# Kernel optimization log

Measured on AMD Instinct MI355X. Metric: run time of the kernel, lower is better.

## Reference

```python
import jax, jax.numpy as jnp
import numpy as np

BS, SL, NN, NE = 8, 100, 200, 600
C = 110; CP1 = C + 1
D = 128          # node_embed_dim
DC = 64          # concept_embed_dim
H = 256          # lstm hidden
VOCAB = 50000
NPROB = 1000
FEAT = 2 + CP1 + DC  # LSTM input dim = 177


def setup_inputs() -> dict:
    key = jax.random.key(0)
    ks = jax.random.split(key, 24)
    f32 = jnp.float32
    p_id = jax.random.randint(ks[0], (BS, SL), 0, NPROB)
    c_id = jax.random.bernoulli(ks[1], 0.1, (BS, SL, CP1)).astype(f32)
    node_id = jax.random.randint(ks[2], (BS, SL, NN), 0, VOCAB)
    edge = jax.random.randint(ks[3], (BS, SL, 2, NE), 0, NN)
    edge_type = jax.random.randint(ks[4], (BS, SL, NE), 0, 8)
    target_c = jax.random.bernoulli(ks[5], 0.05, (BS, SL, CP1)).astype(f32)
    target_c = target_c.at[:, :, 0].set(1.0)  # every step has >=1 target concept
    result = jax.random.bernoulli(ks[6], 0.5, (BS * SL, 1)).astype(f32)
    c_embed = jax.random.bernoulli(ks[7], 0.1, (BS, SL, CP1)).astype(f32)
    cur_result = jax.random.normal(ks[8], (BS, SL, 2), f32)
    # parameters
    node_embed_w = jax.random.normal(ks[9], (VOCAB, D), f32) * 0.02
    edge_embed_w = (jax.random.normal(ks[10], (8, D), f32) * 0.02).at[0].set(0.0)  # padding_idx=0
    ggnn_w = jax.random.normal(ks[11], (4, D, D), f32) * 0.05
    gru_w_ih = jax.random.normal(ks[12], (3 * D, D), f32) * 0.05
    gru_w_hh = jax.random.normal(ks[13], (3 * D, D), f32) * 0.05
    gru_b_ih = jnp.zeros((3 * D,), f32)
    gru_b_hh = jnp.zeros((3 * D,), f32)
    transdim_w = jax.random.normal(ks[14], (DC, D), f32) * 0.05
    concept_embedding = jax.random.normal(ks[15], (CP1, DC), f32) * 0.05
    lstm_w_ih = jax.random.normal(ks[16], (4 * H, FEAT), f32) * 0.05
    lstm_w_hh = jax.random.normal(ks[17], (4 * H, H), f32) * 0.05
    lstm_b_ih = jnp.zeros((4 * H,), f32)
    lstm_b_hh = jnp.zeros((4 * H,), f32)
    pred_w = jax.random.normal(ks[18], (CP1, H), f32) * 0.05
    pred_b = jnp.zeros((CP1,), f32)
    return dict(p_id=p_id, c_id=c_id, node_id=node_id, edge=edge, edge_type=edge_type,
                target_c=target_c, result=result, c_embed=c_embed, cur_result=cur_result,
                node_embed_w=node_embed_w, edge_embed_w=edge_embed_w, ggnn_w=ggnn_w,
                gru_w_ih=gru_w_ih, gru_w_hh=gru_w_hh, gru_b_ih=gru_b_ih, gru_b_hh=gru_b_hh,
                transdim_w=transdim_w, concept_embedding=concept_embedding,
                lstm_w_ih=lstm_w_ih, lstm_w_hh=lstm_w_hh, lstm_b_ih=lstm_b_ih,
                lstm_b_hh=lstm_b_hh, pred_w=pred_w, pred_b=pred_b)


def _forward(p_id, c_id, node_id, edge, edge_type, target_c, result, c_embed, cur_result,
             node_embed_w, edge_embed_w, ggnn_w, gru_w_ih, gru_w_hh, gru_b_ih, gru_b_hh,
             transdim_w, concept_embedding, lstm_w_ih, lstm_w_hh, lstm_b_ih, lstm_b_hh,
             pred_w, pred_b):
    bs, sl = p_id.shape
    N = node_id.shape[2]
    G = bs * sl  # all graphs batched (replaces torch per-sample python loop)
    x = node_embed_w[node_id].reshape(G, N, -1)                       # [G,N,D]
    ew = edge_embed_w[edge_type].mean(-1).reshape(G, -1, 1)           # [G,E,1]
    e = edge.reshape(G, 2, -1)
    src, dst = e[:, 0], e[:, 1]                                       # [G,E]
    flat_dst = (dst + jnp.arange(G)[:, None] * N).reshape(-1)
    d = x.shape[-1]
    # GatedGraphConv, 4 layers: m = x @ W_l, sum-aggregate edge_weight*m[src] at dst, GRUCell update
    for l in range(4):
        m = jnp.einsum('gnd,de->gne', x, ggnn_w[l])
        gathered = jnp.take_along_axis(m, src[:, :, None], axis=1)    # [G,E,D]
        msg = (ew * gathered).reshape(-1, d)
        agg = jax.ops.segment_sum(msg, flat_dst, num_segments=G * N).reshape(G, N, d)
        gi = agg @ gru_w_ih.T + gru_b_ih
        gh = x @ gru_w_hh.T + gru_b_hh
        i_r, i_z, i_n = jnp.split(gi, 3, axis=-1)
        h_r, h_z, h_n = jnp.split(gh, 3, axis=-1)
        r = jax.nn.sigmoid(i_r + h_r)
        z = jax.nn.sigmoid(i_z + h_z)
        n = jnp.tanh(i_n + r * h_n)
        x = (1.0 - z) * n + z * x
    # transdim (node_embed_dim != concept_embed_dim)
    ggnn = jnp.einsum('gnd,cd->gnc', x, transdim_w)                   # [G,N,DC]
    # concept-node attention
    ce = c_embed.reshape(G, -1, 1)                                    # [G,C+1,1]
    query = ce * concept_embedding[None]                              # [G,C+1,DC]
    attn_w = jax.nn.softmax(jnp.einsum('gcd,gnd->gcn', query, ggnn), axis=2)
    attn = jnp.einsum('gcn,gnd->gcd', attn_w, ggnn) * ce
    num = jnp.sum(c_id, axis=2).reshape(G, 1)
    num = jnp.where(num == 0, 1.0, num)
    attn_out = (jnp.sum(attn, axis=1) / num).reshape(bs, sl, -1)
    # LSTM (1 layer, batch_first)
    lstm_in = jnp.concatenate([c_embed, attn_out, cur_result], axis=2)
    hdim = pred_w.shape[1]
    def step(carry, xt):
        h, c = carry
        gates = xt @ lstm_w_ih.T + lstm_b_ih + h @ lstm_w_hh.T + lstm_b_hh
        i, f, g, o = jnp.split(gates, 4, axis=-1)
        c = jax.nn.sigmoid(f) * c + jax.nn.sigmoid(i) * jnp.tanh(g)
        h = jax.nn.sigmoid(o) * jnp.tanh(c)
        return (h, c), h
    init = (jnp.zeros((bs, hdim), lstm_in.dtype), jnp.zeros((bs, hdim), lstm_in.dtype))
    _, hs = jax.lax.scan(step, init, jnp.swapaxes(lstm_in, 0, 1))
    lstm_out = jnp.swapaxes(hs, 0, 1).reshape(G, hdim)
    # prediction + masked BCE-with-logits
    pred = lstm_out @ pred_w.T + pred_b                               # [G,C+1]
    tc = target_c.reshape(G, -1)
    pred1 = jnp.sum(pred * tc, axis=1)
    nc = jnp.sum(tc, axis=1)
    mask = nc > 0
    fp = pred1 / jnp.where(mask, nc, 1.0)
    ft = result.reshape(-1)
    bce = jnp.maximum(fp, 0.0) - fp * ft + jnp.log1p(jnp.exp(-jnp.abs(fp)))
    mf = mask.astype(fp.dtype)
    loss = jnp.sum(bce * mf) / jnp.maximum(jnp.sum(mf), 1.0)
    return loss, jax.nn.sigmoid(fp), ft


def reference(p_id, c_id, node_id, edge, edge_type, target_c, result, c_embed, cur_result,
              node_embed_w, edge_embed_w, ggnn_w, gru_w_ih, gru_w_hh, gru_b_ih, gru_b_hh,
              transdim_w, concept_embedding, lstm_w_ih, lstm_w_hh, lstm_b_ih, lstm_b_hh,
              pred_w, pred_b):
    return _forward(p_id, c_id, node_id, edge, edge_type, target_c, result, c_embed, cur_result,
                    node_embed_w, edge_embed_w, ggnn_w, gru_w_ih, gru_w_hh, gru_b_ih, gru_b_hh,
                    transdim_w, concept_embedding, lstm_w_ih, lstm_w_hh, lstm_b_ih, lstm_b_hh,
                    pred_w, pred_b)
```

## Files before the change

### kernel.cpp

```cpp
#include <hip/hip_runtime.h>
#include <math.h>

static const int BSZ   = 8;
static const int SLN   = 100;
static const int NNODE = 200;
static const int NEDGE = 600;
static const int CP1N  = 111;
static const int DIM   = 128;
static const int DCN   = 64;
static const int HID   = 256;
static const int FEATN = 177;
static const int GN    = 800;
static const int MROW  = 160000;

typedef unsigned short u16;
typedef u16    u16x8  __attribute__((ext_vector_type(8)));
typedef __bf16 bf16x8 __attribute__((ext_vector_type(8)));
typedef __bf16 bf16x2 __attribute__((ext_vector_type(2)));
typedef float  f32x16 __attribute__((ext_vector_type(16)));

#if defined(__has_builtin)
# if __has_builtin(__builtin_amdgcn_fdot2_f32_bf16)
#  define HAVE_FDOT2 1
# else
#  define HAVE_FDOT2 0
# endif
#else
# define HAVE_FDOT2 0
#endif

__device__ __forceinline__ float sigf(float v){ return 1.0f/(1.0f + expf(-v)); }
__device__ __forceinline__ u16 f2bf(float f){
    union { float f; unsigned u; } v; v.f = f;
    unsigned r = v.u + 0x7FFFu + ((v.u >> 16) & 1u);
    return (u16)(r >> 16);
}
__device__ __forceinline__ float bf2f(u16 u){
    union { unsigned u; float f; } v; v.u = ((unsigned)u) << 16;
    return v.f;
}
__device__ __forceinline__ float dot2bf(unsigned w, unsigned h, float acc){
#if HAVE_FDOT2
    return __builtin_amdgcn_fdot2_f32_bf16(__builtin_bit_cast(bf16x2, w),
                                           __builtin_bit_cast(bf16x2, h), acc, false);
#else
    acc += bf2f((u16)(w & 0xffffu)) * bf2f((u16)(h & 0xffffu));
    acc += bf2f((u16)(w >> 16))     * bf2f((u16)(h >> 16));
    return acc;
#endif
}

__device__ __forceinline__ int afrag_slot(int row, int kc8){
    int kcq = kc8 >> 1;
    int pos = (row & 31) + 32*(kc8 & 1);
    return ((row >> 5)*8 + kcq)*64 + (pos ^ kcq);
}

__global__ void k_transpose_w(const float* __restrict__ whh, const float* __restrict__ wih,
                              unsigned* __restrict__ whhP, float* __restrict__ wihT){
    int idx = blockIdx.x*blockDim.x + threadIdx.x;
    const int total1 = 128*1024;
    if (idx < total1){
        int k2 = idx >> 10, j = idx & 1023;
        u16 lo = f2bf(whh[(size_t)j*256 + 2*k2]);
        u16 hi = f2bf(whh[(size_t)j*256 + 2*k2 + 1]);
        whhP[(size_t)k2*1024 + j] = (unsigned)lo | ((unsigned)hi << 16);
    }
    int idx2 = idx - total1;
    const int total2 = FEATN*1024;
    if (idx2 >= 0 && idx2 < total2){
        int k = idx2 >> 10, j = idx2 & 1023;
        wihT[(size_t)k*1024 + j] = wih[(size_t)j*FEATN + k];
    }
}

__global__ void k_convert_w(const float* __restrict__ wih, const float* __restrict__ whh,
                            const float* __restrict__ gw, const float* __restrict__ tw,
                            u16* __restrict__ wihb, u16* __restrict__ whhb,
                            u16* __restrict__ gwTb, u16* __restrict__ twb){
    int idx = blockIdx.x*blockDim.x + threadIdx.x;
    if (idx < 49152){
        wihb[idx] = f2bf(wih[idx]);
    } else if (idx < 98304){
        int t = idx - 49152;
        whhb[t] = f2bf(whh[t]);
    } else if (idx < 163840){
        int t = idx - 98304;
        int l = t >> 14, rem = t & 16383, n = rem >> 7, k = rem & 127;
        gwTb[t] = f2bf(gw[((size_t)l*128 + k)*128 + n]);
    } else if (idx < 172032){
        int t = idx - 163840;
        twb[t] = f2bf(tw[t]);
    }
}

__global__ void __launch_bounds__(256)
k_build_csr(const int* __restrict__ edge, const int* __restrict__ etype,
            const float* __restrict__ eembed,
            int* __restrict__ csr_src, float* __restrict__ csr_w, int* __restrict__ csr_off){
    int g = blockIdx.x; int tid = threadIdx.x;
    __shared__ float tmean[8];
    __shared__ float tpart[8][32];
    __shared__ int cnt[NNODE];
    __shared__ int offs[NNODE+1];
    __shared__ int cur[NNODE];
    {
        int ty = tid >> 5, lane = tid & 31;
        float s = 0.f;
        for (int i = lane; i < DIM; i += 32) s += eembed[ty*DIM + i];
        tpart[ty][lane] = s;
    }
    for (int i = tid; i < NNODE; i += 256) cnt[i] = 0;
    __syncthreads();
    if (tid < 8){
        float s = 0.f;
        for (int i = 0; i < 32; i++) s += tpart[tid][i];
        tmean[tid] = s / (float)DIM;
    }
    for (int e = tid; e < NEDGE; e += 256){
        int dst = edge[((size_t)g*2+1)*NEDGE + e];
        atomicAdd(&cnt[dst], 1);
    }
    __syncthreads();
    if (tid == 0){
        int run = 0;
        for (int i = 0; i < NNODE; i++){ offs[i] = run; run += cnt[i]; }
        offs[NNODE] = run;
    }
    __syncthreads();
    for (int i = tid; i < NNODE; i += 256) cur[i] = offs[i];
    for (int i = tid; i < NNODE+1; i += 256) csr_off[(size_t)g*(NNODE+1)+i] = offs[i];
    __syncthreads();
    for (int e = tid; e < NEDGE; e += 256){
        int dst = edge[((size_t)g*2+1)*NEDGE + e];
        int src = edge[((size_t)g*2+0)*NEDGE + e];
        float w = tmean[etype[(size_t)g*NEDGE + e]];
        int pos = atomicAdd(&cur[dst], 1);
        csr_src[(size_t)g*NEDGE + pos] = src;
        csr_w [(size_t)g*NEDGE + pos] = w;
    }
}

__global__ void k_gather_x(const int* __restrict__ nid, const float4* __restrict__ emb,
                           u16x8* __restrict__ xb){
    const long total = (long)MROW*16;
    for (long c = (long)blockIdx.x*blockDim.x + threadIdx.x; c < total; c += (long)gridDim.x*blockDim.x){
        long row = c >> 4; int p = (int)(c & 15);
        float4 a = emb[(size_t)nid[row]*32 + p*2];
        float4 b = emb[(size_t)nid[row]*32 + p*2 + 1];
        u16x8 v;
        v[0]=f2bf(a.x); v[1]=f2bf(a.y); v[2]=f2bf(a.z); v[3]=f2bf(a.w);
        v[4]=f2bf(b.x); v[5]=f2bf(b.y); v[6]=f2bf(b.z); v[7]=f2bf(b.w);
        xb[c] = v;
    }
}

__global__ void __launch_bounds__(256)
k_mm_scatter(const u16* __restrict__ xb, const u16* __restrict__ gwTb_l,
             const int* __restrict__ csr_src, const float* __restrict__ csr_w,
             const int* __restrict__ csr_off, u16* __restrict__ aggb){
    __shared__ u16 smem[224*128];
    __shared__ int   e_src[NEDGE];
    __shared__ float e_w[NEDGE];
    __shared__ int   offs_s[NNODE+1];
    int g = blockIdx.x;
    int tid = threadIdx.x;
    const u16x8* xg = (const u16x8*)(xb + (size_t)g*NNODE*DIM);
    u16x8* afrag = (u16x8*)smem;
    for (int c = tid; c < 3584; c += 256){
        int row = c >> 4, kc8 = c & 15;
        u16x8 v = {};
        if (row < NNODE) v = xg[row*16 + kc8];
        afrag[afrag_slot(row, kc8)] = v;
    }
    {
        const int*   srcp = csr_src + (size_t)g*NEDGE;
        const float* wp   = csr_w   + (size_t)g*NEDGE;
        const int*   off  = csr_off + (size_t)g*(NNODE+1);
        for (int i = tid; i < NEDGE; i += 256){ e_src[i] = srcp[i]; e_w[i] = wp[i]; }
        for (int i = tid; i <= NNODE; i += 256) offs_s[i] = off[i];
    }
    __syncthreads();
    int w = tid >> 6, lane = tid & 63;
    int nbase = w*32;
    int m = lane & 31, kh = lane >> 5;
    f32x16 acc[7];
    #pragma unroll
    for (int t = 0; t < 7; t++) acc[t] = (f32x16)0.f;
    const u16x8* bp = (const u16x8*)gwTb_l;
    int nrow = nbase + m;
    #pragma unroll
    for (int kc = 0; kc < 8; kc++){
        u16x8 b = bp[nrow*16 + kc*2 + kh];
        #pragma unroll
        for (int mt = 0; mt < 7; mt++){
            u16x8 a = afrag[(mt*8 + kc)*64 + (lane ^ kc)];
            acc[mt] = __builtin_amdgcn_mfma_f32_32x32x16_bf16(
                __builtin_bit_cast(bf16x8, a), __builtin_bit_cast(bf16x8, b), acc[mt], 0, 0, 0);
        }
    }
    __syncthreads();
    #pragma unroll
    for (int mt = 0; mt < 7; mt++){
        #pragma unroll
        for (int r = 0; r < 16; r++){
            int row = mt*32 + (r&3) + 8*(r>>2) + 4*kh;
            int col = nbase + m;
            smem[row*128 + col] = f2bf(acc[mt][r]);
        }
    }
    __syncthreads();
    const unsigned* m32 = (const unsigned*)smem;
    int j2 = tid & 63, rg = tid >> 6;
    unsigned* aggout = (unsigned*)(aggb + (size_t)g*NNODE*DIM);
    for (int i = 0; i < 50; i++){
        int n = rg*50 + i;
        int b0 = offs_s[n], e0 = offs_s[n+1];
        float a0 = 0.f, a1 = 0.f;
        for (int p = b0; p < e0; p++){
            unsigned mv = m32[e_src[p]*64 + j2];
            float w_ = e_w[p];
            a0 += w_ * bf2f((u16)(mv & 0xffffu));
            a1 += w_ * bf2f((u16)(mv >> 16));
        }
        aggout[(size_t)n*64 + j2] = (unsigned)f2bf(a0) | ((unsigned)f2bf(a1) << 16);
    }
}

__global__ void __launch_bounds__(512, 2)
k_gru_mfma(u16* __restrict__ xb, const u16* __restrict__ aggb,
           const u16* __restrict__ wihb, const u16* __restrict__ whhb,
           const float* __restrict__ bih, const float* __restrict__ bhh){
    __shared__ u16x8 afragA[2048];
    __shared__ u16x8 afragX[2048];
    int tid = threadIdx.x;
    long r0 = (long)blockIdx.x * 128;
    const u16x8* aggp = (const u16x8*)aggb;
    const u16x8* xbp  = (const u16x8*)xb;
    for (int c = tid; c < 4096; c += 512){
        int mat = c >> 11, cc = c & 2047;
        int row = cc >> 4, kc8 = cc & 15;
        u16x8 v = (mat ? xbp : aggp)[(r0 + row)*16 + kc8];
        (mat ? afragX : afragA)[afrag_slot(row, kc8)] = v;
    }
    __syncthreads();
    int w = tid >> 6, lane = tid & 63;
    int mtg = w >> 2;
    int cb  = (w & 3) * 32;
    f32x16 acc0[6], acc1[6];
    #pragma unroll
    for (int t = 0; t < 6; t++){ acc0[t] = (f32x16)0.f; acc1[t] = (f32x16)0.f; }
    const u16x8* bi = (const u16x8*)wihb;
    const u16x8* bh = (const u16x8*)whhb;
    int kh = lane >> 5;
    int ncol = cb + (lane & 31);
    #pragma unroll
    for (int kc = 0; kc < 8; kc++){
        int lx = lane ^ kc;
        u16x8 aA0 = afragA[((2*mtg+0)*8 + kc)*64 + lx];
        u16x8 aA1 = afragA[((2*mtg+1)*8 + kc)*64 + lx];
        u16x8 aX0 = afragX[((2*mtg+0)*8 + kc)*64 + lx];
        u16x8 aX1 = afragX[((2*mtg+1)*8 + kc)*64 + lx];
        #pragma unroll
        for (int g3 = 0; g3 < 3; g3++){
            int n = g3*128 + ncol;
            u16x8 b1 = bi[n*16 + kc*2 + kh];
            u16x8 b2 = bh[n*16 + kc*2 + kh];
            acc0[g3]   = __builtin_amdgcn_mfma_f32_32x32x16_bf16(
                __builtin_bit_cast(bf16x8, aA0), __builtin_bit_cast(bf16x8, b1), acc0[g3], 0,0,0);
            acc1[g3]   = __builtin_amdgcn_mfma_f32_32x32x16_bf16(
                __builtin_bit_cast(bf16x8, aA1), __builtin_bit_cast(bf16x8, b1), acc1[g3], 0,0,0);
            acc0[3+g3] = __builtin_amdgcn_mfma_f32_32x32x16_bf16(
                __builtin_bit_cast(bf16x8, aX0), __builtin_bit_cast(bf16x8, b2), acc0[3+g3], 0,0,0);
            acc1[3+g3] = __builtin_amdgcn_mfma_f32_32x32x16_bf16(
                __builtin_bit_cast(bf16x8, aX1), __builtin_bit_cast(bf16x8, b2), acc1[3+g3], 0,0,0);
        }
    }
    int col = cb + (lane & 31);
    float bir = bih[col], biz = bih[col+128], bin = bih[col+256];
    float bhr = bhh[col], bhz = bhh[col+128], bhn = bhh[col+256];
    int kc8c = col >> 3, elc = col & 7;
    #pragma unroll
    for (int mt2 = 0; mt2 < 2; mt2++){
        const f32x16* ac = mt2 ? acc1 : acc0;
        #pragma unroll
        for (int r = 0; r < 16; r++){
            int row = mtg*64 + mt2*32 + (r&3) + 8*(r>>2) + 4*kh;
            u16x8 xv = afragX[afrag_slot(row, kc8c)];
            float xo = bf2f(((const u16*)&xv)[elc]);
            float rr  = sigf(ac[0][r] + bir + ac[3][r] + bhr);
            float zz  = sigf(ac[1][r] + biz + ac[4][r] + bhz);
            float nn_ = tanhf(ac[2][r] + bin + rr*(ac[5][r] + bhn));
            float xn  = (1.f - zz)*nn_ + zz*xo;
            xb[(size_t)(r0 + row)*DIM + col] = f2bf(xn);
        }
    }
}

__global__ void __launch_bounds__(256)
k_transdim(const u16* __restrict__ xb, const u16* __restrict__ twb, u16* __restrict__ out){
    int tid = threadIdx.x;
    int w = tid >> 6, lane = tid & 63;
    int m = lane & 31, kh = lane >> 5;
    long r0 = (long)blockIdx.x * 128;
    const u16x8* xp = (const u16x8*)xb;
    const u16x8* tp = (const u16x8*)twb;
    long rowA = r0 + w*32 + m;
    f32x16 acc[2];
    acc[0] = (f32x16)0.f; acc[1] = (f32x16)0.f;
    #pragma unroll
    for (int kc = 0; kc < 8; kc++){
        u16x8 a = xp[rowA*16 + kc*2 + kh];
        #pragma unroll
        for (int nt = 0; nt < 2; nt++){
            u16x8 b = tp[(nt*32 + m)*16 + kc*2 + kh];
            acc[nt] = __builtin_amdgcn_mfma_f32_32x32x16_bf16(
                __builtin_bit_cast(bf16x8, a), __builtin_bit_cast(bf16x8, b), acc[nt], 0,0,0);
        }
    }
    #pragma unroll
    for (int nt = 0; nt < 2; nt++){
        #pragma unroll
        for (int r = 0; r < 16; r++){
            int row = w*32 + (r&3) + 8*(r>>2) + 4*kh;
            int col = nt*32 + m;
            out[(r0 + row)*DCN + col] = f2bf(acc[nt][r]);
        }
    }
}

__global__ void __launch_bounds__(256)
k_attention(const u16* __restrict__ gout, const float* __restrict__ cemb,
            const float* __restrict__ cid, const float* __restrict__ conc,
            const float* __restrict__ curres, float* __restrict__ lstm_in){
    int g = blockIdx.x; int tid = threadIdx.x;
    int lane = tid & 63, wv = tid >> 6;
    __shared__ float gg[NNODE*65];
    __shared__ float ce_s[CP1N];
    __shared__ float sc[256];
    __shared__ float wredA[4];
    __shared__ float wredB[4];
    __shared__ float part[4][DCN];
    __shared__ float oacc[DCN];
    __shared__ float num_s;
    if (tid < CP1N) ce_s[tid] = cemb[(size_t)g*CP1N + tid];
    if (tid < DCN) oacc[tid] = 0.f;
    for (int i = tid; i < NNODE*DCN; i += 256){
        int n = i >> 6, d = i & 63;
        gg[n*65 + d] = bf2f(gout[(size_t)g*NNODE*DCN + i]);
    }
    {
        float v = (tid < CP1N) ? cid[(size_t)g*CP1N + tid] : 0.f;
        #pragma unroll
        for (int m2 = 32; m2; m2 >>= 1) v += __shfl_xor(v, m2);
        if (lane == 0) wredA[wv] = v;
    }
    __syncthreads();
    if (tid == 0){
        float nm = wredA[0]+wredA[1]+wredA[2]+wredA[3];
        num_s = (nm == 0.f) ? 1.f : nm;
    }
    __syncthreads();
    for (int c = 0; c < CP1N; c++){
        float ce = ce_s[c];
        if (ce == 0.f) continue;
        const float* qc = conc + c*DCN;
        float s = -1e30f;
        if (tid < NNODE){
            float a_ = 0.f;
            const float* gr_ = &gg[tid*65];
            #pragma unroll 16
            for (int d = 0; d < DCN; d++) a_ += qc[d] * gr_[d];
            s = ce * a_;
        }
        float m_ = s;
        #pragma unroll
        for (int m2 = 32; m2; m2 >>= 1) m_ = fmaxf(m_, __shfl_xor(m_, m2));
        if (lane == 0) wredA[wv] = m_;
        __syncthreads();
        float mx = fmaxf(fmaxf(wredA[0], wredA[1]), fmaxf(wredA[2], wredA[3]));
        float e = (tid < NNODE) ? expf(s - mx) : 0.f;
        sc[tid] = e;
        float sum_ = e;
        #pragma unroll
        for (int m2 = 32; m2; m2 >>= 1) sum_ += __shfl_xor(sum_, m2);
        if (lane == 0) wredB[wv] = sum_;
        __syncthreads();
        float inv = ce / (wredB[0]+wredB[1]+wredB[2]+wredB[3]);
        float pa = 0.f;
        for (int n = wv; n < NNODE; n += 4) pa += sc[n] * gg[n*65 + lane];
        part[wv][lane] = pa;
        __syncthreads();
        if (tid < DCN) oacc[tid] += inv * (part[0][tid] + part[1][tid] + part[2][tid] + part[3][tid]);
    }
    __syncthreads();
    if (tid < FEATN){
        float v;
        if      (tid < CP1N)       v = ce_s[tid];
        else if (tid < CP1N+DCN)   v = oacc[tid-CP1N] / num_s;
        else                       v = curres[(size_t)g*2 + (tid-CP1N-DCN)];
        lstm_in[(size_t)g*FEATN + tid] = v;
    }
}

__global__ void __launch_bounds__(256)
k_gi(const float* __restrict__ lstm_in, const float* __restrict__ wihT,
     const float* __restrict__ bih, const float* __restrict__ bhh, float* __restrict__ gi){
    int rb = blockIdx.x;
    int jb = blockIdx.y;
    int tid = threadIdx.x;
    __shared__ float in_s[8][FEATN];
    for (int i = tid; i < 8*FEATN; i += 256){ int r = i/FEATN, k = i%FEATN; in_s[r][k] = lstm_in[((size_t)rb*8+r)*FEATN + k]; }
    __syncthreads();
    int j = jb*256 + tid;
    float acc[8];
    #pragma unroll
    for (int i = 0; i < 8; i++) acc[i] = 0.f;
    for (int k = 0; k < FEATN; k++){
        float w = wihT[(size_t)k*1024 + j];
        #pragma unroll
        for (int i = 0; i < 8; i++) acc[i] += in_s[i][k] * w;
    }
    float b = bih[j] + bhh[j];
    #pragma unroll
    for (int i = 0; i < 8; i++) gi[((size_t)rb*8+i)*1024 + j] = acc[i] + b;
}

static const int WREG = 104;
static const int WL4  = 6;

__global__ void __launch_bounds__(1024)
__attribute__((amdgpu_waves_per_eu(4,4)))
k_lstm(const float* __restrict__ gi, const unsigned* __restrict__ whhP, float* __restrict__ out){
    int b = blockIdx.x; int tid = threadIdx.x;
    __shared__ uint4 ldsw4[WL4][1024];
    __shared__ float gates[1024];
    __shared__ __align__(8) u16 h16[HID];
    unsigned wreg[WREG];
    #pragma unroll
    for (int i = 0; i < WREG; i++) wreg[i] = whhP[(size_t)i*1024 + tid];
    #pragma unroll
    for (int q = 0; q < WL4; q++){
        uint4 v;
        v.x = whhP[(size_t)(WREG + 4*q + 0)*1024 + tid];
        v.y = whhP[(size_t)(WREG + 4*q + 1)*1024 + tid];
        v.z = whhP[(size_t)(WREG + 4*q + 2)*1024 + tid];
        v.w = whhP[(size_t)(WREG + 4*q + 3)*1024 + tid];
        ldsw4[q][tid] = v;
    }
    if (tid < 128) ((unsigned*)h16)[tid] = 0u;
    float c_reg = 0.f;
    int lane = tid & 63;
    __syncthreads();
    float giv = gi[(size_t)b*SLN*1024 + tid];
    for (int t = 0; t < SLN; t++){
        unsigned hv0 = ((const unsigned*)h16)[lane];
        unsigned hv1 = ((const unsigned*)h16)[64 + lane];
        float acc0 = giv, acc1 = 0.f;
        if (t+1 < SLN) giv = gi[((size_t)b*SLN + t + 1)*1024 + tid];
        #pragma unroll
        for (int p = 0; p < 64; p += 2){
            unsigned hpa = (unsigned)__builtin_amdgcn_readlane((int)hv0, p);
            unsigned hpb = (unsigned)__builtin_amdgcn_readlane((int)hv0, p+1);
            acc0 = dot2bf(wreg[p],   hpa, acc0);
            acc1 = dot2bf(wreg[p+1], hpb, acc1);
        }
        #pragma unroll
        for (int p = 64; p < WREG; p += 2){
            unsigned hpa = (unsigned)__builtin_amdgcn_readlane((int)hv1, p - 64);
            unsigned hpb = (unsigned)__builtin_amdgcn_readlane((int)hv1, p - 63);
            acc0 = dot2bf(wreg[p],   hpa, acc0);
            acc1 = dot2bf(wreg[p+1], hpb, acc1);
        }
        #pragma unroll
        for (int q = 0; q < WL4; q++){
            uint4 wv = ldsw4[q][tid];
            int base = WREG + 4*q - 64;
            unsigned h0 = (unsigned)__builtin_amdgcn_readlane((int)hv1, base + 0);
            unsigned h1 = (unsigned)__builtin_amdgcn_readlane((int)hv1, base + 1);
            unsigned h2 = (unsigned)__builtin_amdgcn_readlane((int)hv1, base + 2);
            unsigned h3 = (unsigned)__builtin_amdgcn_readlane((int)hv1, base + 3);
            acc0 = dot2bf(wv.x, h0, acc0);
            acc1 = dot2bf(wv.y, h1, acc1);
            acc0 = dot2bf(wv.z, h2, acc0);
            acc1 = dot2bf(wv.w, h3, acc1);
        }
        gates[tid] = acc0 + acc1;
        __syncthreads();
        if (tid < HID){
            float i_ = sigf(gates[tid]);
            float f_ = sigf(gates[tid+256]);
            float g_ = tanhf(gates[tid+512]);
            float o_ = sigf(gates[tid+768]);
            c_reg = f_*c_reg + i_*g_;
            float h = o_*tanhf(c_reg);
            out[((size_t)b*SLN + t)*HID + tid] = h;
            h16[tid] = f2bf(h);
        }
        __syncthreads();
    }
}

__global__ void __launch_bounds__(128)
k_final(const float* __restrict__ lstm_out, const float* __restrict__ pw, const float* __restrict__ pb,
        const float* __restrict__ tc, const float* __restrict__ result,
        float* __restrict__ out, float* __restrict__ lacc){
    int row = blockIdx.x; int tid = threadIdx.x;
    __shared__ __align__(16) float h_s[HID];
    __shared__ float redv[128], redn[128];
    h_s[tid]       = lstm_out[(size_t)row*HID + tid];
    h_s[tid + 128] = lstm_out[(size_t)row*HID + tid + 128];
    __syncthreads();
    float v = 0.f, n = 0.f;
    if (tid < CP1N){
        float acc = pb[tid];
        const float4* wr = (const float4*)(pw + (size_t)tid*HID);
        const float4* hp = (const float4*)h_s;
        #pragma unroll 8
        for (int k4 = 0; k4 < 64; k4++){
            float4 w = wr[k4]; float4 h4 = hp[k4];
            acc += h4.x*w.x + h4.y*w.y + h4.z*w.z + h4.w*w.w;
        }
        float t = tc[(size_t)row*CP1N + tid];
        v = acc*t; n = t;
    }
    redv[tid] = v; redn[tid] = n;
    __syncthreads();
    for (int s = 64; s > 0; s >>= 1){
        if (tid < s){ redv[tid] += redv[tid+s]; redn[tid] += redn[tid+s]; }
        __syncthreads();
    }
    if (tid == 0){
        float nc = redn[0];
        bool mask = nc > 0.f;
        float fp = redv[0] / (mask ? nc : 1.f);
        float ft = result[row];
        float bce = fmaxf(fp, 0.f) - fp*ft + log1pf(expf(-fabsf(fp)));
        out[1 + row]      = 1.f/(1.f + expf(-fp));
        out[1 + GN + row] = ft;
        if (mask){ atomicAdd(&lacc[0], bce); atomicAdd(&lacc[1], 1.f); }
    }
}

__global__ void k_loss_final(const float* __restrict__ lacc, float* __restrict__ out){
    out[0] = lacc[0] / fmaxf(lacc[1], 1.f);
}

extern "C" void kernel_launch(void* const* d_in, const int* in_sizes, int n_in,
                              void* d_out, int out_size, void* d_ws, size_t ws_size,
                              hipStream_t stream) {
    const float* c_id        = (const float*)d_in[1];
    const int*   node_id     = (const int*)  d_in[2];
    const int*   edge        = (const int*)  d_in[3];
    const int*   etype       = (const int*)  d_in[4];
    const float* target_c    = (const float*)d_in[5];
    const float* result      = (const float*)d_in[6];
    const float* c_embed     = (const float*)d_in[7];
    const float* cur_result  = (const float*)d_in[8];
    const float* node_emb_w  = (const float*)d_in[9];
    const float* edge_emb_w  = (const float*)d_in[10];
    const float* ggnn_w      = (const float*)d_in[11];
    const float* gru_w_ih    = (const float*)d_in[12];
    const float* gru_w_hh    = (const float*)d_in[13];
    const float* gru_b_ih    = (const float*)d_in[14];
    const float* gru_b_hh    = (const float*)d_in[15];
    const float* transdim_w  = (const float*)d_in[16];
    const float* concept     = (const float*)d_in[17];
    const float* lstm_w_ih   = (const float*)d_in[18];
    const float* lstm_w_hh   = (const float*)d_in[19];
    const float* lstm_b_ih   = (const float*)d_in[20];
    const float* lstm_b_hh   = (const float*)d_in[21];
    const float* pred_w      = (const float*)d_in[22];
    const float* pred_b      = (const float*)d_in[23];
    float* out = (float*)d_out;

    char* ws = (char*)d_ws;
    size_t off = 0;
    auto alloc = [&](size_t bytes) -> void* {
        void* p = ws + off;
        off += (bytes + 255) & ~(size_t)255;
        return p;
    };
    u16*      xb       = (u16*)     alloc((size_t)MROW*DIM*2);
    u16*      aggb     = (u16*)     alloc((size_t)MROW*DIM*2);
    int*      csr_src  = (int*)     alloc((size_t)GN*NEDGE*4);
    float*    csr_w    = (float*)   alloc((size_t)GN*NEDGE*4);
    int*      csr_off  = (int*)     alloc((size_t)GN*(NNODE+1)*4);
    float*    lstm_in  = (float*)   alloc((size_t)GN*FEATN*4);
    float*    gi       = (float*)   alloc((size_t)GN*1024*4);
    unsigned* whhP     = (unsigned*)alloc((size_t)128*1024*4);
    float*    wihT     = (float*)   alloc((size_t)FEATN*1024*4);
    float*    lstm_out = (float*)   alloc((size_t)GN*HID*4);
    u16*      wihb     = (u16*)     alloc((size_t)384*128*2);
    u16*      whhb     = (u16*)     alloc((size_t)384*128*2);
    u16*      gwTb     = (u16*)     alloc((size_t)4*128*128*2);
    u16*      twb      = (u16*)     alloc((size_t)DCN*DIM*2);
    float*    lacc     = (float*)   alloc(256);
    u16*      ggnn_out = (u16*)aggb;

    hipMemsetAsync(lacc, 0, 8, stream);
    {
        int total = 128*1024 + FEATN*1024;
        k_transpose_w<<<(total + 255)/256, 256, 0, stream>>>(lstm_w_hh, lstm_w_ih, whhP, wihT);
    }
    k_convert_w<<<672, 256, 0, stream>>>(gru_w_ih, gru_w_hh, ggnn_w, transdim_w, wihb, whhb, gwTb, twb);
    k_build_csr<<<GN, 256, 0, stream>>>(edge, etype, edge_emb_w, csr_src, csr_w, csr_off);
    k_gather_x<<<4096, 256, 0, stream>>>(node_id, (const float4*)node_emb_w, (u16x8*)xb);
    for (int l = 0; l < 4; l++){
        k_mm_scatter<<<GN, 256, 0, stream>>>(xb, gwTb + (size_t)l*DIM*DIM,
                                             csr_src, csr_w, csr_off, aggb);
        k_gru_mfma<<<MROW/128, 512, 0, stream>>>(xb, aggb, wihb, whhb, gru_b_ih, gru_b_hh);
    }
    k_transdim<<<MROW/128, 256, 0, stream>>>(xb, twb, ggnn_out);
    k_attention<<<GN, 256, 0, stream>>>(ggnn_out, c_embed, c_id, concept, cur_result, lstm_in);
    k_gi<<<dim3(100, 4), 256, 0, stream>>>(lstm_in, wihT, lstm_b_ih, lstm_b_hh, gi);
    k_lstm<<<BSZ, 1024, 0, stream>>>(gi, whhP, lstm_out);
    k_final<<<GN, 128, 0, stream>>>(lstm_out, pred_w, pred_b, target_c, result, out, lacc);
    k_loss_final<<<1, 1, 0, stream>>>(lacc, out);
}
```

Measured before the change: 1.314 ms.

## Fuse transdim projection into attention kernel and use fast exp/rcp activations

```diff
diff --git a/kernel.cpp b/kernel.cpp
--- a/kernel.cpp
+++ b/kernel.cpp
@@ -25,11 +25,40 @@
 # else
 #  define HAVE_FDOT2 0
 # endif
+# if __has_builtin(__builtin_amdgcn_exp2f)
+#  define HAVE_EXP2 1
+# else
+#  define HAVE_EXP2 0
+# endif
+# if __has_builtin(__builtin_amdgcn_rcpf)
+#  define HAVE_RCP 1
+# else
+#  define HAVE_RCP 0
+# endif
 #else
 # define HAVE_FDOT2 0
+# define HAVE_EXP2 0
+# define HAVE_RCP 0
 #endif
 
-__device__ __forceinline__ float sigf(float v){ return 1.0f/(1.0f + expf(-v)); }
+static __device__ __forceinline__ float fexp2(float x){
+#if HAVE_EXP2
+    return __builtin_amdgcn_exp2f(x);
+#else
+    return exp2f(x);
+#endif
+}
+static __device__ __forceinline__ float frcp(float x){
+#if HAVE_RCP
+    return __builtin_amdgcn_rcpf(x);
+#else
+    return 1.f/x;
+#endif
+}
+#define LOG2E 1.44269504088896340736f
+static __device__ __forceinline__ float sigf(float v){ return frcp(1.f + fexp2(-LOG2E*v)); }
+static __device__ __forceinline__ float tanh_f(float v){ return 1.f - 2.f*frcp(fexp2(2.f*LOG2E*v) + 1.f); }
+
 __device__ __forceinline__ u16 f2bf(float f){
     union { float f; unsigned u; } v; v.f = f;
     unsigned r = v.u + 0x7FFFu + ((v.u >> 16) & 1u);
@@ -290,7 +319,7 @@
             float xo = bf2f(((const u16*)&xv)[elc]);
             float rr  = sigf(ac[0][r] + bir + ac[3][r] + bhr);
             float zz  = sigf(ac[1][r] + biz + ac[4][r] + bhz);
-            float nn_ = tanhf(ac[2][r] + bin + rr*(ac[5][r] + bhn));
+            float nn_ = tanh_f(ac[2][r] + bin + rr*(ac[5][r] + bhn));
             float xn  = (1.f - zz)*nn_ + zz*xo;
             xb[(size_t)(r0 + row)*DIM + col] = f2bf(xn);
         }
@@ -298,44 +327,13 @@
 }
 
 __global__ void __launch_bounds__(256)
-k_transdim(const u16* __restrict__ xb, const u16* __restrict__ twb, u16* __restrict__ out){
-    int tid = threadIdx.x;
-    int w = tid >> 6, lane = tid & 63;
-    int m = lane & 31, kh = lane >> 5;
-    long r0 = (long)blockIdx.x * 128;
-    const u16x8* xp = (const u16x8*)xb;
-    const u16x8* tp = (const u16x8*)twb;
-    long rowA = r0 + w*32 + m;
-    f32x16 acc[2];
-    acc[0] = (f32x16)0.f; acc[1] = (f32x16)0.f;
-    #pragma unroll
-    for (int kc = 0; kc < 8; kc++){
-        u16x8 a = xp[rowA*16 + kc*2 + kh];
-        #pragma unroll
-        for (int nt = 0; nt < 2; nt++){
-            u16x8 b = tp[(nt*32 + m)*16 + kc*2 + kh];
-            acc[nt] = __builtin_amdgcn_mfma_f32_32x32x16_bf16(
-                __builtin_bit_cast(bf16x8, a), __builtin_bit_cast(bf16x8, b), acc[nt], 0,0,0);
-        }
-    }
-    #pragma unroll
-    for (int nt = 0; nt < 2; nt++){
-        #pragma unroll
-        for (int r = 0; r < 16; r++){
-            int row = w*32 + (r&3) + 8*(r>>2) + 4*kh;
-            int col = nt*32 + m;
-            out[(r0 + row)*DCN + col] = f2bf(acc[nt][r]);
-        }
-    }
-}
-
-__global__ void __launch_bounds__(256)
-k_attention(const u16* __restrict__ gout, const float* __restrict__ cemb,
-            const float* __restrict__ cid, const float* __restrict__ conc,
-            const float* __restrict__ curres, float* __restrict__ lstm_in){
+k_attention(const u16* __restrict__ xb, const u16* __restrict__ twb,
+            const float* __restrict__ cemb, const float* __restrict__ cid,
+            const float* __restrict__ conc, const float* __restrict__ curres,
+            float* __restrict__ lstm_in){
     int g = blockIdx.x; int tid = threadIdx.x;
     int lane = tid & 63, wv = tid >> 6;
-    __shared__ float gg[NNODE*65];
+    __shared__ __align__(16) unsigned char smem_raw[57344];
     __shared__ float ce_s[CP1N];
     __shared__ float sc[256];
     __shared__ float wredA[4];
@@ -343,12 +341,17 @@
     __shared__ float part[4][DCN];
     __shared__ float oacc[DCN];
     __shared__ float num_s;
+    u16x8* afrag = (u16x8*)smem_raw;
+    float* gg    = (float*)smem_raw;
+    const u16x8* xg = (const u16x8*)(xb + (size_t)g*NNODE*DIM);
+    for (int c = tid; c < 3584; c += 256){
+        int row = c >> 4, kc8 = c & 15;
+        u16x8 v = {};
+        if (row < NNODE) v = xg[row*16 + kc8];
+        afrag[afrag_slot(row, kc8)] = v;
+    }
     if (tid < CP1N) ce_s[tid] = cemb[(size_t)g*CP1N + tid];
     if (tid < DCN) oacc[tid] = 0.f;
-    for (int i = tid; i < NNODE*DCN; i += 256){
-        int n = i >> 6, d = i & 63;
-        gg[n*65 + d] = bf2f(gout[(size_t)g*NNODE*DCN + i]);
-    }
     {
         float v = (tid < CP1N) ? cid[(size_t)g*CP1N + tid] : 0.f;
         #pragma unroll
@@ -359,6 +362,33 @@
     if (tid == 0){
         float nm = wredA[0]+wredA[1]+wredA[2]+wredA[3];
         num_s = (nm == 0.f) ? 1.f : nm;
+    }
+    {
+        int ct = wv & 1, rh = wv >> 1;
+        int tb = rh ? 4 : 0, nt = rh ? 3 : 4;
+        int m = lane & 31, kh = lane >> 5;
+        f32x16 acc[4];
+        #pragma unroll
+        for (int t = 0; t < 4; t++) acc[t] = (f32x16)0.f;
+        const u16x8* tp = (const u16x8*)twb;
+        #pragma unroll
+        for (int kc = 0; kc < 8; kc++){
+            u16x8 b = tp[(ct*32 + m)*16 + kc*2 + kh];
+            for (int t = 0; t < nt; t++){
+                u16x8 a = afrag[((tb+t)*8 + kc)*64 + (lane ^ kc)];
+                acc[t] = __builtin_amdgcn_mfma_f32_32x32x16_bf16(
+                    __builtin_bit_cast(bf16x8, a), __builtin_bit_cast(bf16x8, b), acc[t], 0,0,0);
+            }
+        }
+        __syncthreads();
+        for (int t = 0; t < nt; t++){
+            #pragma unroll
+            for (int r = 0; r < 16; r++){
+                int row = (tb+t)*32 + (r&3) + 8*(r>>2) + 4*kh;
+                int col = ct*32 + m;
+                if (row < NNODE) gg[row*65 + col] = acc[t][r];
+            }
+        }
     }
     __syncthreads();
     for (int c = 0; c < CP1N; c++){
@@ -379,7 +409,7 @@
         if (lane == 0) wredA[wv] = m_;
         __syncthreads();
         float mx = fmaxf(fmaxf(wredA[0], wredA[1]), fmaxf(wredA[2], wredA[3]));
-        float e = (tid < NNODE) ? expf(s - mx) : 0.f;
+        float e = (tid < NNODE) ? fexp2(LOG2E*(s - mx)) : 0.f;
         sc[tid] = e;
         float sum_ = e;
         #pragma unroll
@@ -490,10 +520,10 @@
         if (tid < HID){
             float i_ = sigf(gates[tid]);
             float f_ = sigf(gates[tid+256]);
-            float g_ = tanhf(gates[tid+512]);
+            float g_ = tanh_f(gates[tid+512]);
             float o_ = sigf(gates[tid+768]);
             c_reg = f_*c_reg + i_*g_;
-            float h = o_*tanhf(c_reg);
+            float h = o_*tanh_f(c_reg);
             out[((size_t)b*SLN + t)*HID + tid] = h;
             h16[tid] = f2bf(h);
         }
@@ -596,7 +626,6 @@
     u16*      gwTb     = (u16*)     alloc((size_t)4*128*128*2);
     u16*      twb      = (u16*)     alloc((size_t)DCN*DIM*2);
     float*    lacc     = (float*)   alloc(256);
-    u16*      ggnn_out = (u16*)aggb;
 
     hipMemsetAsync(lacc, 0, 8, stream);
     {
@@ -611,8 +640,7 @@
                                              csr_src, csr_w, csr_off, aggb);
         k_gru_mfma<<<MROW/128, 512, 0, stream>>>(xb, aggb, wihb, whhb, gru_b_ih, gru_b_hh);
     }
-    k_transdim<<<MROW/128, 256, 0, stream>>>(xb, twb, ggnn_out);
-    k_attention<<<GN, 256, 0, stream>>>(ggnn_out, c_embed, c_id, concept, cur_result, lstm_in);
+    k_attention<<<GN, 256, 0, stream>>>(xb, twb, c_embed, c_id, concept, cur_result, lstm_in);
     k_gi<<<dim3(100, 4), 256, 0, stream>>>(lstm_in, wihT, lstm_b_ih, lstm_b_hh, gi);
     k_lstm<<<BSZ, 1024, 0, stream>>>(gi, whhP, lstm_out);
     k_final<<<GN, 128, 0, stream>>>(lstm_out, pred_w, pred_b, target_c, result, out, lacc);
```

Result: no change. 1.296 ms (-1.4%).
